# Optimization experiments

Measured on AMD Instinct MI355X. Metric: run time of the kernel, lower is better.

## Reference

```python
import jax, jax.numpy as jnp
import numpy as np

# Constants mirroring FFTGADBase(feature_extractor='none', Npre=2000, block_size=64, overlap=16)
L = 0.24            # diffusion step size l
K_COEF = 0.03       # K = exp(logk), logk = log(0.03) fixed in RGB mode
EPS = 1e-8
BLOCK_SIZE = 64
OVERLAP = 16
NPRE = 2000
FFT_STEPS = 10
VAR_THRESH = 0.1
UNIF_FRAC = 0.7
B, H, W = 2, 1024, 1024
SH, SW = 128, 128


def _g(x, K):
    # Perona-Malik edge-stopping function (repo's g)
    return 1.0 / (1.0 + (x * x) / (K * K))


def _c(feats, K):
    # diffusion coefficients from channel-mean absolute finite differences
    cv = _g(jnp.mean(jnp.abs(feats[:, :, 1:, :] - feats[:, :, :-1, :]), axis=1, keepdims=True), K)
    ch = _g(jnp.mean(jnp.abs(feats[:, :, :, 1:] - feats[:, :, :, :-1]), axis=1, keepdims=True), K)
    return cv, ch  # cv: [B,1,H-1,W], ch: [B,1,H,W-1]


def _diffuse_step(cv, ch, I, l=L):
    # anisotropic diffusion stencil update (transmissions between neighbors)
    dv = I[:, :, 1:, :] - I[:, :, :-1, :]
    dh = I[:, :, :, 1:] - I[:, :, :, :-1]
    tv = l * cv * dv
    th = l * ch * dh
    I = I - jnp.pad(tv, ((0, 0), (0, 0), (1, 0), (0, 0))) + jnp.pad(tv, ((0, 0), (0, 0), (0, 1), (0, 0)))
    I = I - jnp.pad(th, ((0, 0), (0, 0), (0, 0), (1, 0))) + jnp.pad(th, ((0, 0), (0, 0), (0, 0), (0, 1)))
    return I


def _adjust_step(img, source, mask_inv):
    b, c, h, w = img.shape
    sh, sw = source.shape[2], source.shape[3]
    fy, fx = h // sh, w // sw
    # AdaptiveAvgPool2d((sh,sw)) with exact divisor == uniform 8x8 mean pool
    img_ss = img.reshape(b, c, sh, fy, sw, fx).mean(axis=(3, 5))
    ratio_ss = source / (img_ss + EPS)
    ratio_ss = jnp.where(mask_inv, 1.0, ratio_ss)
    # F.interpolate(mode='nearest') with exact multiple == pixel repeat
    ratio = jnp.repeat(jnp.repeat(ratio_ss, fy, axis=2), fx, axis=3)
    return img * ratio


def _avgpool3(x):
    # F.avg_pool2d(x, 3, stride=1, padding=1), count_include_pad=True -> /9 everywhere
    s = jax.lax.reduce_window(x, 0.0, jax.lax.add, (1, 1, 3, 3), (1, 1, 1, 1),
                              [(0, 0), (0, 0), (1, 1), (1, 1)])
    return s / 9.0


def _uniform_regions(cv, ch):
    cv_var = _avgpool3(cv ** 2) - _avgpool3(cv) ** 2
    ch_var = _avgpool3(ch ** 2) - _avgpool3(ch) ** 2
    hm = min(cv_var.shape[2], ch_var.shape[2])
    wm = min(cv_var.shape[3], ch_var.shape[3])
    return (cv_var[:, :, :hm, :wm] < VAR_THRESH) & (ch_var[:, :, :hm, :wm] < VAR_THRESH)


def _fft_block(block, cv_b, ch_b):
    # Closed-form multi-step uniform-coefficient diffusion in the Fourier domain:
    # eigenvalue of one explicit diffusion step on periodic grid, raised to FFT_STEPS.
    cv_m = cv_b.mean(axis=(1, 2, 3), keepdims=True)  # [B,1,1,1]
    ch_m = ch_b.mean(axis=(1, 2, 3), keepdims=True)
    bh, bw = block.shape[-2], block.shape[-1]
    fy = jnp.arange(bh, dtype=jnp.float32)[:, None]
    fx = jnp.arange(bw // 2 + 1, dtype=jnp.float32)[None, :]
    lam = (1.0 - 2.0 * L * cv_m * (1.0 - jnp.cos(2.0 * jnp.pi * fy / bh))
               - 2.0 * L * ch_m * (1.0 - jnp.cos(2.0 * jnp.pi * fx / bw)))
    Fb = jnp.fft.rfft2(block)
    return jnp.fft.irfft2(Fb * (lam ** FFT_STEPS), s=(bh, bw)).astype(block.dtype)


def _fft_diffuse(depth, cv, ch, ur):
    b, c, h, w = depth.shape
    h_cv, w_cv = cv.shape[2], cv.shape[3]
    h_ch, w_ch = ch.shape[2], ch.shape[3]
    step = BLOCK_SIZE - OVERLAP
    for y in range(0, h, step):
        for x in range(0, w, step):
            ye, xe = min(y + BLOCK_SIZE, h), min(x + BLOCK_SIZE, w)
            cye, cxe = min(ye - 1, h_cv), min(xe, w_cv)
            hye, hxe = min(ye, h_ch), min(xe - 1, w_ch)
            if y >= cye or x >= cxe or y >= hye or x >= hxe:
                continue
            uye, uxe = min(ye, ur.shape[2]), min(xe, ur.shape[3])
            if y >= uye or x >= uxe:
                continue
            old = depth[:, :, y:ye, x:xe]
            new = _fft_block(old, cv[:, :, y:cye, x:cxe], ch[:, :, y:hye, x:hxe])
            unif = ur[:, :, y:uye, x:uxe].astype(jnp.float32).mean(axis=(1, 2, 3))
            apply_fft = (unif > UNIF_FRAC)[:, None, None, None]
            bh, bw = ye - y, xe - x
            by = jnp.ones((bh,), dtype=jnp.float32)
            if y > 0:
                n = min(OVERLAP, bh)
                by = by.at[:n].set(jnp.arange(n, dtype=jnp.float32) / OVERLAP)
            bx = jnp.ones((bw,), dtype=jnp.float32)
            if x > 0:
                n = min(OVERLAP, bw)
                bx = bx.at[:n].set(jnp.arange(n, dtype=jnp.float32) / OVERLAP)
            blend = by[:, None] * bx[None, :]
            merged = old * (1.0 - blend) + new * blend  # at (0,0) blend==1 -> direct write, as in torch
            merged = jnp.where(apply_fft, merged, old)
            depth = depth.at[:, :, y:ye, x:xe].set(merged)
    return depth


def _diffuse(img, guide, source, mask_inv):
    # RGB mode: guide_feats = cat([guide, img], 1); K = exp(logk) = 0.03
    feats = jnp.concatenate([guide, img], axis=1)
    cv, ch = _c(feats, K_COEF)
    ur = _uniform_regions(cv, ch)
    # Npre section runs under torch.no_grad()
    img0 = jax.lax.stop_gradient(img)
    cv0 = jax.lax.stop_gradient(cv)
    ch0 = jax.lax.stop_gradient(ch)
    img0 = _fft_diffuse(img0, cv0, ch0, ur)

    def body(I, _):
        I = _diffuse_step(cv0, ch0, I)
        I = _adjust_step(I, jax.lax.stop_gradient(source), mask_inv)
        return I, None

    y_pred, _ = jax.lax.scan(body, img0, None, length=min(500, NPRE))
    return y_pred, cv, ch


def setup_inputs() -> dict:
    key = jax.random.key(0)
    k1, k2, k3, k4 = jax.random.split(key, 4)
    guide = jax.random.normal(k1, (B, 3, H, W), dtype=jnp.float32)
    # keep depths safely > deps=0.1 so the shift branch is statically off
    source = jax.random.uniform(k2, (B, 1, SH, SW), dtype=jnp.float32) + 0.5
    mask_lr = jax.random.uniform(k3, (B, 1, SH, SW), dtype=jnp.float32)
    y_bicubic = jnp.repeat(jnp.repeat(source, H // SH, axis=2), W // SW, axis=3) \
                + 0.05 * jax.random.normal(k4, (B, 1, H, W), dtype=jnp.float32)
    return {"guide": guide, "source": source, "mask_lr": mask_lr, "y_bicubic": y_bicubic}


def reference(guide, source, mask_lr, y_bicubic):
    mask_inv = mask_lr < 0.5
    y_pred, cv, ch = _diffuse(y_bicubic, guide, source, mask_inv)
    return y_pred, cv, ch
```

## Files before the change

### kernel.cpp

```cpp
#include <hip/hip_runtime.h>

#define HH 1024
#define WW 1024
#define HW 1048576
#define NBLK 22

__device__ __forceinline__ float aload(const float* p)
{
    return __uint_as_float(__hip_atomic_load((const unsigned int*)p,
                           __ATOMIC_RELAXED, __HIP_MEMORY_SCOPE_AGENT));
}
__device__ __forceinline__ void astore(float* p, float v)
{
    __hip_atomic_store((unsigned int*)p, __float_as_uint(v),
                       __ATOMIC_RELAXED, __HIP_MEMORY_SCOPE_AGENT);
}

__global__ __launch_bounds__(256) void coeff_kernel(
    const float* __restrict__ guide, const float* __restrict__ img,
    float* __restrict__ cv, float* __restrict__ ch)
{
    int x = blockIdx.x * 256 + threadIdx.x;
    int y = blockIdx.y;
    int b = blockIdx.z;
    const float* g0 = guide + (size_t)b * 3 * HW;
    const float* im = img + (size_t)b * HW;
    int p = y * WW + x;
    float f0 = g0[p], f1 = g0[HW + p], f2 = g0[2 * HW + p], f3 = im[p];
    const float KK = 0.03f * 0.03f;
    if (y < HH - 1) {
        int q = p + WW;
        float s = fabsf(g0[q] - f0) + fabsf(g0[HW + q] - f1)
                + fabsf(g0[2 * HW + q] - f2) + fabsf(im[q] - f3);
        float t = s * 0.25f;
        cv[(size_t)b * 1023 * 1024 + p] = 1.0f / (1.0f + t * t / KK);
    }
    if (x < WW - 1) {
        int q = p + 1;
        float s = fabsf(g0[q] - f0) + fabsf(g0[HW + q] - f1)
                + fabsf(g0[2 * HW + q] - f2) + fabsf(im[q] - f3);
        float t = s * 0.25f;
        ch[(size_t)b * 1024 * 1023 + y * 1023 + x] = 1.0f / (1.0f + t * t / KK);
    }
}

__device__ __forceinline__ float block_reduce(float v, float* tmp)
{
    #pragma unroll
    for (int off = 32; off > 0; off >>= 1) v += __shfl_down(v, off);
    __syncthreads();
    if ((threadIdx.x & 63) == 0) tmp[threadIdx.x >> 6] = v;
    __syncthreads();
    return tmp[0] + tmp[1] + tmp[2] + tmp[3];
}

__global__ __launch_bounds__(256) void stats_kernel(
    const float* __restrict__ cv, const float* __restrict__ ch,
    float* __restrict__ cvmA, float* __restrict__ chmA, float* __restrict__ unifA)
{
    int iy = blockIdx.x, ix = blockIdx.y, b = blockIdx.z;
    int y0 = iy * 48, x0 = ix * 48;
    int ye = min(y0 + 64, HH), xe = min(x0 + 64, WW);
    int bh = ye - y0, bw = xe - x0;
    const float* cvb = cv + (size_t)b * 1023 * 1024;
    const float* chb = ch + (size_t)b * 1024 * 1023;
    int tid = threadIdx.x;

    int cnt_cv = (bh - 1) * bw;
    float s_cv = 0.f;
    for (int k = tid; k < cnt_cv; k += 256) {
        int r = k / bw, c = k - r * bw;
        s_cv += cvb[(y0 + r) * 1024 + x0 + c];
    }
    int cnt_ch = bh * (bw - 1);
    float s_ch = 0.f;
    for (int k = tid; k < cnt_ch; k += 256) {
        int r = k / (bw - 1), c = k - r * (bw - 1);
        s_ch += chb[(y0 + r) * 1023 + x0 + c];
    }
    int uh = min(ye, 1023) - y0, uw = min(xe, 1023) - x0;
    int cnt_u = uh * uw;
    float s_u = 0.f;
    for (int k = tid; k < cnt_u; k += 256) {
        int r = k / uw, c = k - r * uw;
        int py = y0 + r, px = x0 + c;
        float a1 = 0.f, a2 = 0.f;
        #pragma unroll
        for (int dy = -1; dy <= 1; ++dy)
            #pragma unroll
            for (int dx = -1; dx <= 1; ++dx) {
                int yy = py + dy, xx = px + dx;
                if (yy >= 0 && yy < 1023 && xx >= 0 && xx < 1024) {
                    float v = cvb[yy * 1024 + xx]; a1 += v; a2 += v * v;
                }
            }
        float va = a2 * (1.f / 9.f) - (a1 * (1.f / 9.f)) * (a1 * (1.f / 9.f));
        float b1 = 0.f, b2 = 0.f;
        #pragma unroll
        for (int dy = -1; dy <= 1; ++dy)
            #pragma unroll
            for (int dx = -1; dx <= 1; ++dx) {
                int yy = py + dy, xx = px + dx;
                if (yy >= 0 && yy < 1024 && xx >= 0 && xx < 1023) {
                    float v = chb[yy * 1023 + xx]; b1 += v; b2 += v * v;
                }
            }
        float vb = b2 * (1.f / 9.f) - (b1 * (1.f / 9.f)) * (b1 * (1.f / 9.f));
        s_u += (va < 0.1f && vb < 0.1f) ? 1.f : 0.f;
    }

    __shared__ float tmp[4];
    float t_cv = block_reduce(s_cv, tmp);
    float t_ch = block_reduce(s_ch, tmp);
    float t_u  = block_reduce(s_u, tmp);
    if (tid == 0) {
        int bi = (b * NBLK + iy) * NBLK + ix;
        cvmA[bi]  = t_cv / (float)cnt_cv;
        chmA[bi]  = t_ch / (float)cnt_ch;
        unifA[bi] = t_u / (float)cnt_u;
    }
}

__global__ __launch_bounds__(256) void fftblk_kernel(
    float* __restrict__ depth,
    const float* __restrict__ cvmA, const float* __restrict__ chmA,
    const float* __restrict__ unifA, int d, int iy_lo)
{
    int iy = iy_lo + (int)blockIdx.x;
    int ix = d - 2 * iy;
    int b = blockIdx.y;
    int bi = (b * NBLK + iy) * NBLK + ix;
    if (!(unifA[bi] > 0.7f)) return;

    int y0 = iy * 48, x0 = ix * 48;
    int bh = min(64, HH - y0), bw = min(64, WW - x0);
    int npix = bh * bw;
    int bwm = bw - 1, bhm = bh - 1;
    int lw = (bw == 64) ? 6 : 4;
    float av = 0.24f * cvmA[bi];
    float ah = 0.24f * chmA[bi];

    __shared__ float bufA[4096], bufB[4096], bufO[4096];
    float* cur = bufA;
    float* nxt = bufB;
    int tid = threadIdx.x;
    float* gbase = depth + (size_t)b * HW + y0 * WW + x0;

    for (int idx = tid; idx < npix; idx += 256) {
        int i = idx >> lw, j = idx & bwm;
        float v = gbase[i * WW + j];
        cur[idx] = v; bufO[idx] = v;
    }
    __syncthreads();

    for (int it = 0; it < 10; ++it) {
        for (int idx = tid; idx < npix; idx += 256) {
            int i = idx >> lw, j = idx & bwm;
            float c  = cur[idx];
            float up = cur[(((i - 1) & bhm) << lw) | j];
            float dn = cur[(((i + 1) & bhm) << lw) | j];
            float lf = cur[(i << lw) | ((j - 1) & bwm)];
            float rt = cur[(i << lw) | ((j + 1) & bwm)];
            nxt[idx] = c + av * (up + dn - 2.f * c) + ah * (lf + rt - 2.f * c);
        }
        __syncthreads();
        float* t = cur; cur = nxt; nxt = t;
    }

    const float inv16 = 1.f / 16.f;
    for (int idx = tid; idx < npix; idx += 256) {
        int i = idx >> lw, j = idx & bwm;
        float wy = (y0 > 0 && i < 16) ? (float)i * inv16 : 1.f;
        float wx = (x0 > 0 && j < 16) ? (float)j * inv16 : 1.f;
        float w = wy * wx;
        gbase[i * WW + j] = bufO[idx] * (1.f - w) + cur[idx] * w;
    }
}

__global__ __launch_bounds__(256) void fftblk_group(
    float* __restrict__ depth,
    const float* __restrict__ cvmA, const float* __restrict__ chmA,
    const float* __restrict__ unifA, unsigned int* __restrict__ ftags,
    int base)
{
    int rem = base + (int)blockIdx.x;
    int iy = 0, ix = 0;
    for (int d = 0; d < 64; ++d) {
        int lo = (d > 21) ? ((d - 20) >> 1) : 0;
        int hi = ((d >> 1) < 21) ? (d >> 1) : 21;
        int wd = hi - lo + 1;
        if (rem < wd) { iy = lo + rem; ix = d - 2 * iy; break; }
        rem -= wd;
    }
    int b = blockIdx.y;
    int bi = (b * NBLK + iy) * NBLK + ix;
    int tid = threadIdx.x;

    {
        bool act = false; int di = 0, dj = 0;
        if (tid == 0) { act = (ix > 0);            di = iy;     dj = ix - 1; }
        if (tid == 1) { act = (iy > 0 && ix > 0);  di = iy - 1; dj = ix - 1; }
        if (tid == 2) { act = (iy > 0);            di = iy - 1; dj = ix;     }
        if (tid == 3) { act = (iy > 0 && ix < 21); di = iy - 1; dj = ix + 1; }
        if (tid < 4 && act) {
            const unsigned int* tp = ftags + (((b * NBLK + di) * NBLK + dj) << 4);
            int guard = 0;
            while (__hip_atomic_load(tp, __ATOMIC_RELAXED,
                                     __HIP_MEMORY_SCOPE_AGENT) < 1u) {
                if (++guard > (1 << 20)) break;
                __builtin_amdgcn_s_sleep(2);
            }
        }
    }
    __syncthreads();

    bool active = (unifA[bi] > 0.7f);
    if (active) {
        int y0 = iy * 48, x0 = ix * 48;
        int bh = min(64, HH - y0), bw = min(64, WW - x0);
        int npix = bh * bw;
        int bwm = bw - 1, bhm = bh - 1;
        int lw = (bw == 64) ? 6 : 4;
        float av = 0.24f * cvmA[bi];
        float ah = 0.24f * chmA[bi];

        __shared__ float bufA[4096], bufB[4096], bufO[4096];
        float* cur = bufA;
        float* nxt = bufB;
        float* gbase = depth + (size_t)b * HW + y0 * WW + x0;

        float tmp[16];
        #pragma unroll
        for (int k = 0; k < 16; ++k) {
            int idx = tid + k * 256;
            if (idx < npix)
                tmp[k] = aload(gbase + (idx >> lw) * WW + (idx & bwm));
        }
        #pragma unroll
        for (int k = 0; k < 16; ++k) {
            int idx = tid + k * 256;
            if (idx < npix) { cur[idx] = tmp[k]; bufO[idx] = tmp[k]; }
        }
        __syncthreads();

        for (int it = 0; it < 10; ++it) {
            for (int idx = tid; idx < npix; idx += 256) {
                int i = idx >> lw, j = idx & bwm;
                float c  = cur[idx];
                float up = cur[(((i - 1) & bhm) << lw) | j];
                float dn = cur[(((i + 1) & bhm) << lw) | j];
                float lf = cur[(i << lw) | ((j - 1) & bwm)];
                float rt = cur[(i << lw) | ((j + 1) & bwm)];
                nxt[idx] = c + av * (up + dn - 2.f * c) + ah * (lf + rt - 2.f * c);
            }
            __syncthreads();
            float* t = cur; cur = nxt; nxt = t;
        }

        const float inv16 = 1.f / 16.f;
        for (int idx = tid; idx < npix; idx += 256) {
            int i = idx >> lw, j = idx & bwm;
            float wy = (y0 > 0 && i < 16) ? (float)i * inv16 : 1.f;
            float wx = (x0 > 0 && j < 16) ? (float)j * inv16 : 1.f;
            float w = wy * wx;
            astore(gbase + i * WW + j, bufO[idx] * (1.f - w) + cur[idx] * w);
        }
        asm volatile("s_waitcnt vmcnt(0)" ::: "memory");
    }
    __syncthreads();
    if (tid == 0)
        __hip_atomic_store(ftags + (bi << 4), 1u, __ATOMIC_RELAXED,
                           __HIP_MEMORY_SCOPE_AGENT);
}

__global__ __launch_bounds__(256, 4) void iter_kernel(
    const float* __restrict__ Iin, float* __restrict__ Iout,
    const float* __restrict__ cv, const float* __restrict__ ch,
    const float* __restrict__ source, const float* __restrict__ mask)
{
    const int w = blockIdx.x;
    const int xcd = w & 7, j = w >> 3;
    const int grb = xcd * 32 + (j >> 2);
    const int b  = grb >> 7;
    const int r0 = (grb & 127) * 8;
    const int c0 = (j & 3) * 256;
    const int tid = threadIdx.x;
    __shared__ float sI[10][258];
    const float* Ib  = Iin + (size_t)b * HW;
    const float* cvb = cv + (size_t)b * 1023 * 1024;
    const float* chb = ch + (size_t)b * 1024 * 1023;

    for (int k = tid; k < 10 * 258; k += 256) {
        int r = k / 258, c = k - r * 258;
        int gy = r0 - 1 + r, gx = c0 - 1 + c;
        float v = 0.f;
        if (gy >= 0 && gy < HH && gx >= 0 && gx < WW) v = Ib[gy * WW + gx];
        sI[r][c] = v;
    }

    const int gx = c0 + tid;
    float cvv[9];
    #pragma unroll
    for (int k = 0; k < 9; ++k) {
        int gr = r0 - 1 + k;
        cvv[k] = (gr >= 0 && gr < 1023) ? cvb[gr * 1024 + gx] : 0.f;
    }
    float chl[8], chh[8];
    #pragma unroll
    for (int k = 0; k < 8; ++k) {
        int rr = r0 + k;
        chh[k] = (gx < 1023) ? chb[rr * 1023 + gx] : 0.f;
        chl[k] = (gx > 0)    ? chb[rr * 1023 + gx - 1] : 0.f;
    }
    __syncthreads();

    float o[8];
    #pragma unroll
    for (int r = 0; r < 8; ++r) {
        float c  = sI[r + 1][tid + 1];
        float up = sI[r][tid + 1], dn = sI[r + 2][tid + 1];
        float lf = sI[r + 1][tid], rt = sI[r + 1][tid + 2];
        o[r] = c + 0.24f * ( cvv[r + 1] * (dn - c) - cvv[r] * (c - up)
                           + chh[r] * (rt - c)     - chl[r] * (c - lf) );
    }

    float colsum = 0.f;
    #pragma unroll
    for (int r = 0; r < 8; ++r) colsum += o[r];
    colsum += __shfl_xor(colsum, 1);
    colsum += __shfl_xor(colsum, 2);
    colsum += __shfl_xor(colsum, 4);
    float mean = colsum * (1.0f / 64.0f);

    int sy = r0 >> 3;
    int sx = (c0 >> 3) + (tid >> 3);
    int sidx = b * 128 * 128 + sy * 128 + sx;
    float ratio = (mask[sidx] < 0.5f) ? 1.0f : source[sidx] / (mean + 1e-8f);

    float* Ob = Iout + (size_t)b * HW;
    #pragma unroll
    for (int r = 0; r < 8; ++r)
        Ob[(r0 + r) * WW + c0 + tid] = o[r] * ratio;
}

__global__ __launch_bounds__(256, 1) void iter500_strip(
    float* __restrict__ depth,
    const float* __restrict__ cv, const float* __restrict__ ch,
    const float* __restrict__ source, const float* __restrict__ mask,
    float* __restrict__ rowbuf,
    unsigned int* __restrict__ tags,
    int niter)
{
    const int s   = blockIdx.x;
    const int b   = s >> 7;
    const int rb  = s & 127;
    const int r0  = rb * 8;
    const int tid = threadIdx.x;
    const int w   = tid >> 6;
    const int l   = tid & 63;
    const int gx0 = (w << 8) + (l << 2);
    const int swz = (w << 8) + l;

    __shared__ float sE[2][3][2][8];

    float* gdep = depth + (size_t)b * HW;

    float o[8][4];
    #pragma unroll
    for (int r = 0; r < 8; ++r) {
        float4 v = *(const float4*)(gdep + (size_t)(r0 + r) * WW + gx0);
        o[r][0] = v.x; o[r][1] = v.y; o[r][2] = v.z; o[r][3] = v.w;
    }
    unsigned int* mytag = tags + ((s * 4 + w) << 4);
    {
        float* dT = rowbuf + ((size_t)s * 2 + 0) * 1024 + swz;
        float* dB = rowbuf + ((size_t)s * 2 + 1) * 1024 + swz;
        #pragma unroll
        for (int c = 0; c < 4; ++c) { astore(dT + (c << 6), o[0][c]);
                                      astore(dB + (c << 6), o[7][c]); }
        asm volatile("s_waitcnt vmcnt(0)" ::: "memory");
        if (l == 0)
            __hip_atomic_store(mytag, 1u, __ATOMIC_RELAXED, __HIP_MEMORY_SCOPE_AGENT);
    }

    const float* cvb = cv + (size_t)b * 1023 * 1024;
    const float* chb = ch + (size_t)b * 1024 * 1023;
    float cvv[9][4];
    #pragma unroll
    for (int k = 0; k < 9; ++k) {
        int gr = r0 - 1 + k;
        #pragma unroll
        for (int c = 0; c < 4; ++c)
            cvv[k][c] = (gr >= 0 && gr < 1023) ? cvb[(size_t)gr * 1024 + gx0 + c] : 0.f;
    }
    float chh[8][4], chl0[8];
    #pragma unroll
    for (int k = 0; k < 8; ++k) {
        int rr = r0 + k;
        #pragma unroll
        for (int c = 0; c < 4; ++c)
            chh[k][c] = (gx0 + c < 1023) ? chb[(size_t)rr * 1023 + gx0 + c] : 0.f;
        chl0[k] = (gx0 > 0) ? chb[(size_t)rr * 1023 + gx0 - 1] : 0.f;
    }
    int sidx = b * 128 * 128 + rb * 128 + (gx0 >> 3);
    float sval = source[sidx];
    bool  adj  = (mask[sidx] >= 0.5f);

    const unsigned int* tagT = tags + ((((rb > 0   ? s - 1 : s) * 4) + w) << 4);
    const unsigned int* tagB = tags + ((((rb < 127 ? s + 1 : s) * 4) + w) << 4);

    for (int it = 0; it < niter; ++it) {
        const int p = it & 1;
        const int q = p ^ 1;

        if (l == 63 && w < 3) {
            #pragma unroll
            for (int r = 0; r < 8; ++r) sE[p][w][0][r] = o[r][3];
        }
        if (l == 0 && w > 0) {
            #pragma unroll
            for (int r = 0; r < 8; ++r) sE[p][w - 1][1][r] = o[r][0];
        }
        __syncthreads();

        float lfS[8], rtS[8];
        int wl = (w > 0) ? w - 1 : 0;
        int wr = (w < 3) ? w : 0;
        #pragma unroll
        for (int r = 0; r < 8; ++r) {
            float a  = __shfl(o[r][3], l - 1);
            float bq = __shfl(o[r][0], l + 1);
            lfS[r] = (l == 0)  ? ((w > 0) ? sE[p][wl][0][r] : 0.f) : a;
            rtS[r] = (l == 63) ? ((w < 3) ? sE[p][wr][1][r] : 0.f) : bq;
        }

        float n[8][4];
        float cs = 0.f;
        #pragma unroll
        for (int r = 1; r < 7; ++r) {
            #pragma unroll
            for (int c = 0; c < 4; ++c) {
                float cen = o[r][c];
                float up = o[r - 1][c];
                float dn = o[r + 1][c];
                float lf = (c == 0) ? lfS[r] : o[r][c - 1];
                float rt = (c == 3) ? rtS[r] : o[r][c + 1];
                float cl = (c == 0) ? chl0[r] : chh[r][c - 1];
                float v = cen + 0.24f * ( cvv[r + 1][c] * (dn - cen)
                                        - cvv[r][c]     * (cen - up)
                                        + chh[r][c]     * (rt - cen)
                                        - cl            * (cen - lf) );
                n[r][c] = v; cs += v;
            }
        }

        {
            unsigned int target = (unsigned int)(it + 1);
            bool active = (l == 0) ? (rb > 0) : ((l == 1) ? (rb < 127) : false);
            if (active) {
                const unsigned int* pp = (l == 0) ? tagT : tagB;
                int guard = 0;
                while (__hip_atomic_load(pp, __ATOMIC_RELAXED,
                                         __HIP_MEMORY_SCOPE_AGENT) < target) {
                    if (++guard > (1 << 18)) break;
                    __builtin_amdgcn_s_sleep(1);
                }
            }
        }
        asm volatile("" ::: "memory");

        float ht[4] = {0.f, 0.f, 0.f, 0.f}, hb[4] = {0.f, 0.f, 0.f, 0.f};
        if (rb > 0) {
            const float* srcp = rowbuf + (((size_t)p * 256 + (s - 1)) * 2 + 1) * 1024 + swz;
            #pragma unroll
            for (int c = 0; c < 4; ++c) ht[c] = aload(srcp + (c << 6));
        }
        if (rb < 127) {
            const float* srcp = rowbuf + (((size_t)p * 256 + (s + 1)) * 2 + 0) * 1024 + swz;
            #pragma unroll
            for (int c = 0; c < 4; ++c) hb[c] = aload(srcp + (c << 6));
        }

        #pragma unroll
        for (int c = 0; c < 4; ++c) {
            float cen = o[0][c];
            float up = ht[c], dn = o[1][c];
            float lf = (c == 0) ? lfS[0] : o[0][c - 1];
            float rt = (c == 3) ? rtS[0] : o[0][c + 1];
            float cl = (c == 0) ? chl0[0] : chh[0][c - 1];
            float v = cen + 0.24f * ( cvv[1][c] * (dn - cen) - cvv[0][c] * (cen - up)
                                    + chh[0][c] * (rt - cen) - cl * (cen - lf) );
            n[0][c] = v; cs += v;
        }
        #pragma unroll
        for (int c = 0; c < 4; ++c) {
            float cen = o[7][c];
            float up = o[6][c], dn = hb[c];
            float lf = (c == 0) ? lfS[7] : o[7][c - 1];
            float rt = (c == 3) ? rtS[7] : o[7][c + 1];
            float cl = (c == 0) ? chl0[7] : chh[7][c - 1];
            float v = cen + 0.24f * ( cvv[8][c] * (dn - cen) - cvv[7][c] * (cen - up)
                                    + chh[7][c] * (rt - cen) - cl * (cen - lf) );
            n[7][c] = v; cs += v;
        }

        cs += __shfl_xor(cs, 1);
        float mean  = cs * (1.0f / 64.0f);
        float ratio = adj ? sval / (mean + 1e-8f) : 1.0f;
        #pragma unroll
        for (int r = 0; r < 8; ++r)
            #pragma unroll
            for (int c = 0; c < 4; ++c) o[r][c] = n[r][c] * ratio;

        {
            float* dT = rowbuf + (((size_t)q * 256 + s) * 2 + 0) * 1024 + swz;
            float* dB = rowbuf + (((size_t)q * 256 + s) * 2 + 1) * 1024 + swz;
            #pragma unroll
            for (int c = 0; c < 4; ++c) { astore(dT + (c << 6), o[0][c]);
                                          astore(dB + (c << 6), o[7][c]); }
        }
        asm volatile("s_waitcnt vmcnt(0)" ::: "memory");
        if (l == 0)
            __hip_atomic_store(mytag, (unsigned int)(it + 2),
                               __ATOMIC_RELAXED, __HIP_MEMORY_SCOPE_AGENT);
    }

    #pragma unroll
    for (int r = 0; r < 8; ++r) {
        float4 v;
        v.x = o[r][0]; v.y = o[r][1]; v.z = o[r][2]; v.w = o[r][3];
        *(float4*)(gdep + (size_t)(r0 + r) * WW + gx0) = v;
    }
}

extern "C" void kernel_launch(void* const* d_in, const int* in_sizes, int n_in,
                              void* d_out, int out_size, void* d_ws, size_t ws_size,
                              hipStream_t stream)
{
    (void)in_sizes; (void)n_in; (void)out_size; (void)ws_size;
    const float* guide  = (const float*)d_in[0];
    const float* source = (const float*)d_in[1];
    const float* mask   = (const float*)d_in[2];
    const float* ybic   = (const float*)d_in[3];

    float* out   = (float*)d_out;
    float* ypred = out;
    float* cv    = out + 2097152;
    float* ch    = out + 2097152 + 2095104;

    float* wsf    = (float*)d_ws;
    float* dbuf   = wsf;
    float* rowbuf = wsf;
    unsigned int* itags = (unsigned int*)(wsf + 1048576);
    unsigned int* ftags = itags + 16384;
    float* cvmA   = wsf + 2097152;
    float* chmA   = cvmA + 2 * NBLK * NBLK;
    float* unifA  = chmA + 2 * NBLK * NBLK;

    static int persist_ok = -1;
    static int fft_ok = -1;
    static int fgs[16], nfg = 0;
    if (persist_ok < 0) {
        int dev = 0;
        (void)hipGetDevice(&dev);
        hipDeviceProp_t prop;
        int nCU = 0;
        if (hipGetDeviceProperties(&prop, dev) == hipSuccess)
            nCU = prop.multiProcessorCount;
        int nb = 0;
        hipError_t e = hipOccupancyMaxActiveBlocksPerMultiprocessor(
            &nb, iter500_strip, 256, 0);
        persist_ok = (e == hipSuccess && nCU > 0 && nb * nCU >= 256) ? 1 : 0;

        int nb2 = 0;
        hipError_t e2 = hipOccupancyMaxActiveBlocksPerMultiprocessor(
            &nb2, fftblk_group, 256, 0);
        fft_ok = 0;
        if (e2 == hipSuccess && nCU > 0) {
            int capb = (nb2 * nCU) / 2 - 16;
            if (capb >= 64) {
                nfg = 0;
                int start = 0, cnt = 0;
                bool ok = true;
                for (int d = 0; d < 64; ++d) {
                    int lo = (d > 21) ? ((d - 20) >> 1) : 0;
                    int hi = ((d >> 1) < 21) ? (d >> 1) : 21;
                    int wd = hi - lo + 1;
                    if (cnt + wd > capb) {
                        if (nfg >= 15) { ok = false; break; }
                        fgs[nfg * 2] = start; fgs[nfg * 2 + 1] = cnt;
                        ++nfg; start += cnt; cnt = 0;
                    }
                    cnt += wd;
                }
                if (ok && cnt > 0) { fgs[nfg * 2] = start; fgs[nfg * 2 + 1] = cnt; ++nfg; }
                fft_ok = ok ? 1 : 0;
            }
        }
    }

    coeff_kernel<<<dim3(4, HH, 2), 256, 0, stream>>>(guide, ybic, cv, ch);
    stats_kernel<<<dim3(NBLK, NBLK, 2), 256, 0, stream>>>(cv, ch, cvmA, chmA, unifA);
    hipMemcpyAsync(ypred, ybic, (size_t)2 * HW * sizeof(float),
                   hipMemcpyDeviceToDevice, stream);
    hipMemsetAsync(itags, 0, 2 * 16384 * sizeof(unsigned int), stream);

    if (fft_ok) {
        for (int g = 0; g < nfg; ++g)
            fftblk_group<<<dim3(fgs[g * 2 + 1], 2), 256, 0, stream>>>(
                ypred, cvmA, chmA, unifA, ftags, fgs[g * 2]);
    } else {
        for (int d = 0; d <= 3 * (NBLK - 1); ++d) {
            int lo = (d > NBLK - 1) ? (d - NBLK + 2) / 2 : 0;
            int hi = (d / 2 < NBLK - 1) ? d / 2 : NBLK - 1;
            if (lo > hi) continue;
            fftblk_kernel<<<dim3(hi - lo + 1, 2), 256, 0, stream>>>(
                ypred, cvmA, chmA, unifA, d, lo);
        }
    }

    if (persist_ok) {
        iter500_strip<<<dim3(256), 256, 0, stream>>>(
            ypred, cv, ch, source, mask, rowbuf, itags, 500);
    } else {
        for (int i = 0; i < 500; ++i) {
            const float* src = (i & 1) ? dbuf : ypred;
            float*       dst = (i & 1) ? ypred : dbuf;
            iter_kernel<<<dim3(1024), 256, 0, stream>>>(
                src, dst, cv, ch, source, mask);
        }
    }
}
```

Before: 2.413 ms.

## Keep FFT-diffusion block tiles in registers and exchange only halos through LDS

The per-block periodic diffusion (10 steps on a 64x64 or 16x16 tile) now keeps each thread's 4x4 (or 1x1) sub-tile in registers. Only the edge rows and columns go through double-buffered shared-memory halo arrays. This replaces full-tile ping-pong LDS buffers and the index math per pixel, cutting LDS traffic and the original-copy buffer. It adds register pressure and more complex indexing for the wraparound and partial-tile cases.

```diff
diff --git a/kernel.cpp b/kernel.cpp
--- a/kernel.cpp
+++ b/kernel.cpp
@@ -218,53 +218,83 @@
     if (active) {
         int y0 = iy * 48, x0 = ix * 48;
         int bh = min(64, HH - y0), bw = min(64, WW - x0);
-        int npix = bh * bw;
-        int bwm = bw - 1, bhm = bh - 1;
-        int lw = (bw == 64) ? 6 : 4;
+        const int RH = bh >> 4;
+        const int RW = bw >> 4;
         float av = 0.24f * cvmA[bi];
         float ah = 0.24f * chmA[bi];
 
-        __shared__ float bufA[4096], bufB[4096], bufO[4096];
-        float* cur = bufA;
-        float* nxt = bufB;
+        __shared__ float rT[2][16][64];
+        __shared__ float rB[2][16][64];
+        __shared__ float cL[2][16][64];
+        __shared__ float cR[2][16][64];
+
+        const int ty = tid >> 4, tx = tid & 15;
         float* gbase = depth + (size_t)b * HW + y0 * WW + x0;
 
-        float tmp[16];
-        #pragma unroll
-        for (int k = 0; k < 16; ++k) {
-            int idx = tid + k * 256;
-            if (idx < npix)
-                tmp[k] = aload(gbase + (idx >> lw) * WW + (idx & bwm));
-        }
-        #pragma unroll
-        for (int k = 0; k < 16; ++k) {
-            int idx = tid + k * 256;
-            if (idx < npix) { cur[idx] = tmp[k]; bufO[idx] = tmp[k]; }
-        }
-        __syncthreads();
+        float cur[4][4], orig[4][4];
+        #pragma unroll
+        for (int r = 0; r < 4; ++r)
+            #pragma unroll
+            for (int c = 0; c < 4; ++c)
+                if (r < RH && c < RW) {
+                    float v = aload(gbase + (RH * ty + r) * WW + RW * tx + c);
+                    cur[r][c] = v; orig[r][c] = v;
+                }
 
         for (int it = 0; it < 10; ++it) {
-            for (int idx = tid; idx < npix; idx += 256) {
-                int i = idx >> lw, j = idx & bwm;
-                float c  = cur[idx];
-                float up = cur[(((i - 1) & bhm) << lw) | j];
-                float dn = cur[(((i + 1) & bhm) << lw) | j];
-                float lf = cur[(i << lw) | ((j - 1) & bwm)];
-                float rt = cur[(i << lw) | ((j + 1) & bwm)];
-                nxt[idx] = c + av * (up + dn - 2.f * c) + ah * (lf + rt - 2.f * c);
-            }
+            const int p = it & 1;
+            #pragma unroll
+            for (int c = 0; c < 4; ++c)
+                if (c < RW) {
+                    rT[p][ty][RW * tx + c] = cur[0][c];
+                    rB[p][ty][RW * tx + c] = (RH == 4) ? cur[3][c] : cur[0][c];
+                }
+            #pragma unroll
+            for (int r = 0; r < 4; ++r)
+                if (r < RH) {
+                    cL[p][tx][RH * ty + r] = cur[r][0];
+                    cR[p][tx][RH * ty + r] = (RW == 4) ? cur[r][3] : cur[r][0];
+                }
             __syncthreads();
-            float* t = cur; cur = nxt; nxt = t;
+
+            float nxt[4][4];
+            #pragma unroll
+            for (int r = 0; r < 4; ++r)
+                #pragma unroll
+                for (int c = 0; c < 4; ++c)
+                    if (r < RH && c < RW) {
+                        float ce = cur[r][c];
+                        float up = (r > 0) ? cur[r - 1][c]
+                                           : rB[p][(ty - 1) & 15][RW * tx + c];
+                        float dn = rT[p][(ty + 1) & 15][RW * tx + c];
+                        if (r + 1 < 4) { if (r + 1 < RH) dn = cur[r + 1][c]; }
+                        float lf = (c > 0) ? cur[r][c - 1]
+                                           : cR[p][(tx - 1) & 15][RH * ty + r];
+                        float rt = cL[p][(tx + 1) & 15][RH * ty + r];
+                        if (c + 1 < 4) { if (c + 1 < RW) rt = cur[r][c + 1]; }
+                        nxt[r][c] = ce + av * (up + dn - 2.f * ce)
+                                       + ah * (lf + rt - 2.f * ce);
+                    }
+            #pragma unroll
+            for (int r = 0; r < 4; ++r)
+                #pragma unroll
+                for (int c = 0; c < 4; ++c)
+                    if (r < RH && c < RW) cur[r][c] = nxt[r][c];
         }
 
         const float inv16 = 1.f / 16.f;
-        for (int idx = tid; idx < npix; idx += 256) {
-            int i = idx >> lw, j = idx & bwm;
-            float wy = (y0 > 0 && i < 16) ? (float)i * inv16 : 1.f;
-            float wx = (x0 > 0 && j < 16) ? (float)j * inv16 : 1.f;
-            float w = wy * wx;
-            astore(gbase + i * WW + j, bufO[idx] * (1.f - w) + cur[idx] * w);
-        }
+        #pragma unroll
+        for (int r = 0; r < 4; ++r)
+            #pragma unroll
+            for (int c = 0; c < 4; ++c)
+                if (r < RH && c < RW) {
+                    int i = RH * ty + r, j = RW * tx + c;
+                    float wy = (y0 > 0 && i < 16) ? (float)i * inv16 : 1.f;
+                    float wx = (x0 > 0 && j < 16) ? (float)j * inv16 : 1.f;
+                    float w = wy * wx;
+                    astore(gbase + i * WW + j,
+                           orig[r][c] * (1.f - w) + cur[r][c] * w);
+                }
         asm volatile("s_waitcnt vmcnt(0)" ::: "memory");
     }
     __syncthreads();
```

Result: slower. 2.612 ms (+8.3%).
